# Kernel optimization log

Hardware: AMD Instinct MI355X
Metric: run time of the kernel (lower is better)

## Reference

```python
import jax, jax.numpy as jnp
import numpy as np

EMBED = 768
HEADS = 12
HEAD_DIM = EMBED // HEADS
HIDDEN = 4 * EMBED


def layer_norm(x, gamma, beta, eps=1e-5):
    mu = jnp.mean(x, axis=-1, keepdims=True)
    var = jnp.var(x, axis=-1, keepdims=True)
    return (x - mu) * jax.lax.rsqrt(var + eps) * gamma + beta


def setup_inputs() -> dict:
    key = jax.random.key(0)
    ks = jax.random.split(key, 10)
    B, N, C = 64, 577, EMBED
    s_in = 1.0 / np.sqrt(C)
    s_hid = 1.0 / np.sqrt(HIDDEN)
    return {
        "x": jax.random.normal(ks[0], (B, N, C), jnp.float32),
        "ln1_g": jnp.ones((C,), jnp.float32),
        "ln1_b": jnp.zeros((C,), jnp.float32),
        "w_qkv": jax.random.normal(ks[1], (C, 3 * C), jnp.float32) * s_in,  # no bias (qkv_bias=False)
        "w_proj": jax.random.normal(ks[2], (C, C), jnp.float32) * s_in,
        "b_proj": jnp.zeros((C,), jnp.float32),
        "ln2_g": jnp.ones((C,), jnp.float32),
        "ln2_b": jnp.zeros((C,), jnp.float32),
        "w_fc1": jax.random.normal(ks[3], (C, HIDDEN), jnp.float32) * s_in,
        "b_fc1": jnp.zeros((HIDDEN,), jnp.float32),
        "w_fc2": jax.random.normal(ks[4], (HIDDEN, C), jnp.float32) * s_hid,
        "b_fc2": jnp.zeros((C,), jnp.float32),
    }


def reference(x, ln1_g, ln1_b, w_qkv, w_proj, b_proj, ln2_g, ln2_b, w_fc1, b_fc1, w_fc2, b_fc2):
    B, N, C = x.shape
    # --- attention branch (pre-norm) ---
    h = layer_norm(x, ln1_g, ln1_b)
    qkv = (h @ w_qkv).reshape(B, N, 3, HEADS, HEAD_DIM)
    q = jnp.transpose(qkv[:, :, 0], (0, 2, 1, 3))  # [B,H,N,D]
    k = jnp.transpose(qkv[:, :, 1], (0, 2, 1, 3))
    v = jnp.transpose(qkv[:, :, 2], (0, 2, 1, 3))
    scale = HEAD_DIM ** -0.5
    att = jax.nn.softmax(jnp.einsum("bhnd,bhmd->bhnm", q, k) * scale, axis=-1)
    o = jnp.einsum("bhnm,bhmd->bhnd", att, v)
    o = jnp.transpose(o, (0, 2, 1, 3)).reshape(B, N, C)
    x = x + (o @ w_proj + b_proj)
    # --- MLP branch (pre-norm) ---
    h = layer_norm(x, ln2_g, ln2_b)
    h = jax.nn.gelu(h @ w_fc1 + b_fc1, approximate=False)
    x = x + (h @ w_fc2 + b_fc2)
    return x
```

## Files before the change

kernel.cpp:

```cpp
#include <hip/hip_runtime.h>
#include <hip/hip_bf16.h>
#include <math.h>

using bf16 = __hip_bfloat16;
typedef __attribute__((ext_vector_type(8))) short short8;
typedef __attribute__((ext_vector_type(4))) float f32x4;

#define NSEQ   577
#define NBATCH 64
#define NTOK   36928
#define NHEADS 12
#define HDIM   64
#define NP     640
#define CEMB   768
#define CHID   3072
#define NBH    (NBATCH*NHEADS)

__device__ __forceinline__ bf16 f2bf(float v){ return __float2bfloat16(v); }

__device__ __forceinline__ float gelu_f(float x) {
    float x3 = x * x * x;
    float y = 1.5957691216057308f * (x + 0.044715f * x3);
    float e = __expf(y);
    float t = 1.0f - 2.0f / (e + 1.0f);
    return 0.5f * x * (1.0f + t);
}

#define GLOAD_LDS16(gaddr, laddr) \
  __builtin_amdgcn_global_load_lds((__attribute__((address_space(1))) const void*)(gaddr), \
                                   (__attribute__((address_space(3))) void*)(laddr), 16, 0, 0)

__global__ __launch_bounds__(256) void transpose_w(const float* __restrict__ src,
                                                   bf16* __restrict__ dst, int R, int C) {
    long idx = (long)blockIdx.x * 256 + threadIdx.x;
    long total = (long)R * C;
    if (idx < total) {
        int r = (int)(idx / C);
        int c = (int)(idx - (long)r * C);
        dst[(long)c * R + r] = f2bf(src[idx]);
    }
}

__global__ __launch_bounds__(256) void ln_kernel(const float* __restrict__ x,
                                                 const float* __restrict__ gamma,
                                                 const float* __restrict__ beta,
                                                 bf16* __restrict__ out) {
    int row = blockIdx.x;
    const float* xr = x + (size_t)row * CEMB;
    int tid = threadIdx.x;
    float v0 = xr[tid], v1 = xr[tid + 256], v2 = xr[tid + 512];
    float s = v0 + v1 + v2;
    #pragma unroll
    for (int o = 32; o > 0; o >>= 1) s += __shfl_down(s, o);
    __shared__ float red[4];
    if ((tid & 63) == 0) red[tid >> 6] = s;
    __syncthreads();
    float mean = (red[0] + red[1] + red[2] + red[3]) * (1.0f / CEMB);
    float d0 = v0 - mean, d1 = v1 - mean, d2 = v2 - mean;
    float q = d0*d0 + d1*d1 + d2*d2;
    #pragma unroll
    for (int o = 32; o > 0; o >>= 1) q += __shfl_down(q, o);
    __shared__ float red2[4];
    if ((tid & 63) == 0) red2[tid >> 6] = q;
    __syncthreads();
    float var = (red2[0] + red2[1] + red2[2] + red2[3]) * (1.0f / CEMB);
    float rs = rsqrtf(var + 1e-5f);
    bf16* orow = out + (size_t)row * CEMB;
    orow[tid]       = f2bf(d0 * rs * gamma[tid]       + beta[tid]);
    orow[tid + 256] = f2bf(d1 * rs * gamma[tid + 256] + beta[tid + 256]);
    orow[tid + 512] = f2bf(d2 * rs * gamma[tid + 512] + beta[tid + 512]);
}

__global__ __launch_bounds__(256) void flash_attn(const bf16* __restrict__ qg,
                                                  const bf16* __restrict__ kg,
                                                  const bf16* __restrict__ vtg,
                                                  bf16* __restrict__ og) {
    const int tid = threadIdx.x, lane = tid & 63, w = tid >> 6;
    const int fr = lane & 15, fh = lane >> 4;
    const int bh = blockIdx.y;
    const int q0 = blockIdx.x * 128;
    const int wr = w * 32;

    __shared__ bf16 Ks[64 * 64];
    __shared__ bf16 Vs[64 * 64];
    __shared__ bf16 Ps[128 * 64];

    const bf16* qb = qg  + (size_t)bh * NP * HDIM;
    const bf16* kb = kg  + (size_t)bh * NP * HDIM;
    const bf16* vb = vtg + (size_t)bh * HDIM * NP;

    short8 qa[2][2];
    #pragma unroll
    for (int mi = 0; mi < 2; mi++)
        #pragma unroll
        for (int ks = 0; ks < 2; ks++)
            qa[mi][ks] = *reinterpret_cast<const short8*>(
                qb + (size_t)(q0 + wr + mi * 16 + fr) * HDIM + ks * 32 + fh * 8);

    f32x4 od[2][4] = {};
    float m_run[2][4], l_run[2][4];
    #pragma unroll
    for (int mi = 0; mi < 2; mi++)
        #pragma unroll
        for (int r = 0; r < 4; r++) { m_run[mi][r] = -1e30f; l_run[mi][r] = 0.f; }

    for (int t = 0; t < NP / 64; t++) {
        const int kb0 = t * 64;
        __syncthreads();
        {
            const bf16* src = kb + (size_t)kb0 * HDIM;
            GLOAD_LDS16(src + w * 512 + lane * 8,        Ks + w * 512);
            GLOAD_LDS16(src + 2048 + w * 512 + lane * 8, Ks + 2048 + w * 512);
        }
        {
            int d0 = w * 8;
            GLOAD_LDS16(vb + (size_t)(d0 + (lane >> 3)) * NP + kb0 + (lane & 7) * 8,
                        Vs + d0 * 64);
            d0 = 32 + w * 8;
            GLOAD_LDS16(vb + (size_t)(d0 + (lane >> 3)) * NP + kb0 + (lane & 7) * 8,
                        Vs + d0 * 64);
        }
        __syncthreads();

        f32x4 sacc[2][4] = {};
        short8 kf[4][2];
        #pragma unroll
        for (int n = 0; n < 4; n++)
            #pragma unroll
            for (int ks = 0; ks < 2; ks++)
                kf[n][ks] = *reinterpret_cast<const short8*>(&Ks[(n * 16 + fr) * 64 + ks * 32 + fh * 8]);
        #pragma unroll
        for (int mi = 0; mi < 2; mi++)
            #pragma unroll
            for (int n = 0; n < 4; n++)
                #pragma unroll
                for (int ks = 0; ks < 2; ks++)
                    sacc[mi][n] = __builtin_amdgcn_mfma_f32_16x16x32_bf16(qa[mi][ks], kf[n][ks], sacc[mi][n], 0, 0, 0);

        #pragma unroll
        for (int mi = 0; mi < 2; mi++) {
            float sv[4][4];
            float tm[4] = {-1e30f, -1e30f, -1e30f, -1e30f};
            #pragma unroll
            for (int n = 0; n < 4; n++) {
                int col = kb0 + n * 16 + fr;
                bool valid = col < NSEQ;
                #pragma unroll
                for (int r = 0; r < 4; r++) {
                    float s = sacc[mi][n][r] * 0.125f;
                    sv[n][r] = valid ? s : -1e30f;
                    tm[r] = fmaxf(tm[r], sv[n][r]);
                }
            }
            #pragma unroll
            for (int r = 0; r < 4; r++) {
                #pragma unroll
                for (int o = 1; o < 16; o <<= 1) tm[r] = fmaxf(tm[r], __shfl_xor(tm[r], o));
                float mn = fmaxf(m_run[mi][r], tm[r]);
                float sc = __expf(m_run[mi][r] - mn);
                m_run[mi][r] = mn;
                float ps = 0.f;
                #pragma unroll
                for (int n = 0; n < 4; n++) {
                    float e = __expf(sv[n][r] - mn);
                    sv[n][r] = e; ps += e;
                }
                #pragma unroll
                for (int o = 1; o < 16; o <<= 1) ps += __shfl_xor(ps, o);
                l_run[mi][r] = l_run[mi][r] * sc + ps;
                #pragma unroll
                for (int n2 = 0; n2 < 4; n2++) od[mi][n2][r] *= sc;
            }
            #pragma unroll
            for (int n = 0; n < 4; n++)
                #pragma unroll
                for (int r = 0; r < 4; r++)
                    Ps[(wr + mi * 16 + fh * 4 + r) * 64 + n * 16 + fr] = f2bf(sv[n][r]);
        }
        __syncthreads();

        short8 pa[2][2], vf[4][2];
        #pragma unroll
        for (int mi = 0; mi < 2; mi++)
            #pragma unroll
            for (int ks = 0; ks < 2; ks++)
                pa[mi][ks] = *reinterpret_cast<const short8*>(&Ps[(wr + mi * 16 + fr) * 64 + ks * 32 + fh * 8]);
        #pragma unroll
        for (int n2 = 0; n2 < 4; n2++)
            #pragma unroll
            for (int ks = 0; ks < 2; ks++)
                vf[n2][ks] = *reinterpret_cast<const short8*>(&Vs[(n2 * 16 + fr) * 64 + ks * 32 + fh * 8]);
        #pragma unroll
        for (int mi = 0; mi < 2; mi++)
            #pragma unroll
            for (int n2 = 0; n2 < 4; n2++)
                #pragma unroll
                for (int ks = 0; ks < 2; ks++)
                    od[mi][n2] = __builtin_amdgcn_mfma_f32_16x16x32_bf16(pa[mi][ks], vf[n2][ks], od[mi][n2], 0, 0, 0);
    }

    const int b = bh / NHEADS, hh = bh - b * NHEADS;
    #pragma unroll
    for (int mi = 0; mi < 2; mi++)
        #pragma unroll
        for (int r = 0; r < 4; r++) {
            int qrow = q0 + wr + mi * 16 + fh * 4 + r;
            if (qrow < NSEQ) {
                float inv = 1.f / l_run[mi][r];
                #pragma unroll
                for (int n2 = 0; n2 < 4; n2++)
                    og[((size_t)(b * NSEQ + qrow)) * CEMB + hh * HDIM + n2 * 16 + fr] =
                        f2bf(od[mi][n2][r] * inv);
            }
        }
}

#define MODE_QKV  1
#define MODE_PROJ 3
#define MODE_FC1  4
#define MODE_FC2  5

struct GemmParams {
    const bf16* A;
    const bf16* Bt;
    int M, N, K;
    int Mreal;
    float* Cf;
    bf16* Cb;
    const float* bias;
    const float* resid;
    bf16* qb; bf16* kb; bf16* vtb;
};

template<int MODE>
__global__ __launch_bounds__(256) void gemm128(GemmParams p) {
    __shared__ bf16 AsBuf[2][128 * 32];
    __shared__ bf16 BsBuf[2][128 * 32];
    const int tid  = threadIdx.x;
    const int lane = tid & 63;
    const int w    = tid >> 6;

    const int gx = gridDim.x, gy = gridDim.y;
    const int nwg = gx * gy;
    const int orig = blockIdx.y * gx + blockIdx.x;
    const int q8 = nwg >> 3, r8 = nwg & 7;
    const int xcd = orig & 7, oid = orig >> 3;
    const int lin2 = ((xcd < r8) ? xcd * (q8 + 1) : r8 * (q8 + 1) + (xcd - r8) * q8) + oid;
    const int bm = (lin2 / gy) * 128;
    const int bn = (lin2 % gy) * 128;

    const int Kd = p.K;
    const int wr = (w >> 1) * 64;
    const int wc = (w & 1) * 64;
    const int fr = lane & 15;
    const int fk = (lane >> 4) * 8;
    const int idx0 = w * 64 + lane;
    const int idx1 = idx0 + 256;
    const int r0 = idx0 >> 2, c0 = (idx0 & 3) * 8;
    const int r1 = idx1 >> 2, c1 = (idx1 & 3) * 8;

    const bf16* aS0 = p.A  + (size_t)(bm + r0) * Kd + c0;
    const bf16* aS1 = p.A  + (size_t)(bm + r1) * Kd + c1;
    const bf16* bS0 = p.Bt + (size_t)(bn + r0) * Kd + c0;
    const bf16* bS1 = p.Bt + (size_t)(bn + r1) * Kd + c1;

    f32x4 acc[4][4] = {};

    bf16 *Ac = AsBuf[0], *An = AsBuf[1];
    bf16 *Bc = BsBuf[0], *Bn = BsBuf[1];

    auto stage = [&](bf16* Ad, bf16* Bd) {
        GLOAD_LDS16(aS0, Ad + (size_t)w * 512);
        GLOAD_LDS16(aS1, Ad + (size_t)(w + 4) * 512);
        GLOAD_LDS16(bS0, Bd + (size_t)w * 512);
        GLOAD_LDS16(bS1, Bd + (size_t)(w + 4) * 512);
        aS0 += 32; aS1 += 32; bS0 += 32; bS1 += 32;
    };
    auto compute = [&](const bf16* Ad, const bf16* Bd) {
        short8 a[4], b[4];
        #pragma unroll
        for (int m = 0; m < 4; m++)
            a[m] = *reinterpret_cast<const short8*>(&Ad[(wr + m * 16 + fr) * 32 + fk]);
        #pragma unroll
        for (int n = 0; n < 4; n++)
            b[n] = *reinterpret_cast<const short8*>(&Bd[(wc + n * 16 + fr) * 32 + fk]);
        #pragma unroll
        for (int m = 0; m < 4; m++)
            #pragma unroll
            for (int n = 0; n < 4; n++)
                acc[m][n] = __builtin_amdgcn_mfma_f32_16x16x32_bf16(a[m], b[n], acc[m][n], 0, 0, 0);
    };

    const int T = Kd >> 5;
    stage(Ac, Bc);
    __syncthreads();
    for (int t = 1; t < T; ++t) {
        stage(An, Bn);
        compute(Ac, Bc);
        __syncthreads();
        bf16* tp;
        tp = Ac; Ac = An; An = tp;
        tp = Bc; Bc = Bn; Bn = tp;
    }
    compute(Ac, Bc);

    const int fq = (lane >> 4) * 4;
    const int colw = bn + wc;

    if (MODE == MODE_QKV) {
        const int which = colw / CEMB;
        const int hh = (colw - which * CEMB) >> 6;
        #pragma unroll
        for (int m = 0; m < 4; m++)
        #pragma unroll
        for (int r = 0; r < 4; r++) {
            int row = bm + wr + m * 16 + fq + r;
            if (row < p.Mreal) {
                int b2 = row / NSEQ;
                int n2 = row - b2 * NSEQ;
                size_t bh = (size_t)b2 * NHEADS + hh;
                if (which == 0) {
                    bf16* dst = p.qb + (bh * NP + n2) * HDIM + fr;
                    #pragma unroll
                    for (int n = 0; n < 4; n++) dst[n * 16] = f2bf(acc[m][n][r]);
                } else if (which == 1) {
                    bf16* dst = p.kb + (bh * NP + n2) * HDIM + fr;
                    #pragma unroll
                    for (int n = 0; n < 4; n++) dst[n * 16] = f2bf(acc[m][n][r]);
                } else {
                    bf16* dst = p.vtb + (bh * HDIM + fr) * NP + n2;
                    #pragma unroll
                    for (int n = 0; n < 4; n++) dst[(size_t)n * 16 * NP] = f2bf(acc[m][n][r]);
                }
            }
        }
    } else if (MODE == MODE_FC1) {
        const float* bp = p.bias + colw + fr;
        float bb[4];
        #pragma unroll
        for (int n = 0; n < 4; n++) bb[n] = bp[n * 16];
        #pragma unroll
        for (int m = 0; m < 4; m++)
        #pragma unroll
        for (int r = 0; r < 4; r++) {
            int row = bm + wr + m * 16 + fq + r;
            if (row < p.Mreal) {
                bf16* crow = p.Cb + (size_t)row * p.N + colw + fr;
                #pragma unroll
                for (int n = 0; n < 4; n++)
                    crow[n * 16] = f2bf(gelu_f(acc[m][n][r] + bb[n]));
            }
        }
    } else {
        const float* bp = p.bias + colw + fr;
        float bb[4];
        #pragma unroll
        for (int n = 0; n < 4; n++) bb[n] = bp[n * 16];
        #pragma unroll
        for (int m = 0; m < 4; m++)
        #pragma unroll
        for (int r = 0; r < 4; r++) {
            int row = bm + wr + m * 16 + fq + r;
            if (row < p.Mreal) {
                float* crow = p.Cf + (size_t)row * p.N + colw + fr;
                const float* rrow = p.resid + (size_t)row * p.N + colw + fr;
                #pragma unroll
                for (int n = 0; n < 4; n++)
                    crow[n * 16] = acc[m][n][r] + bb[n] + rrow[n * 16];
            }
        }
    }
}

extern "C" void kernel_launch(void* const* d_in, const int* in_sizes, int n_in,
                              void* d_out, int out_size, void* d_ws, size_t ws_size,
                              hipStream_t stream) {
    const float* x      = (const float*)d_in[0];
    const float* ln1_g  = (const float*)d_in[1];
    const float* ln1_b  = (const float*)d_in[2];
    const float* w_qkv  = (const float*)d_in[3];
    const float* w_proj = (const float*)d_in[4];
    const float* b_proj = (const float*)d_in[5];
    const float* ln2_g  = (const float*)d_in[6];
    const float* ln2_b  = (const float*)d_in[7];
    const float* w_fc1  = (const float*)d_in[8];
    const float* b_fc1  = (const float*)d_in[9];
    const float* w_fc2  = (const float*)d_in[10];
    const float* b_fc2  = (const float*)d_in[11];
    float* out = (float*)d_out;

    char* ws = (char*)d_ws;
    auto al = [](size_t b){ return (b + 255) & ~(size_t)255; };
    size_t off = 0;
    auto take = [&](size_t b)->char* { char* p = ws + off; off += al(b); return p; };

    bf16* wqkvT  = (bf16*)take((size_t)2304 * 768 * 2);
    bf16* wprojT = (bf16*)take((size_t)768 * 768 * 2);
    bf16* wfc1T  = (bf16*)take((size_t)3072 * 768 * 2);
    bf16* wfc2T  = (bf16*)take((size_t)768 * 3072 * 2);
    bf16* h      = (bf16*)take((size_t)(NTOK + 128) * CEMB * 2);
    bf16* o      = (bf16*)take((size_t)(NTOK + 128) * CEMB * 2);
    size_t fixedEnd = off;

    const size_t qkvB = (size_t)NBH * NP * HDIM * 2;
    bf16* q_c  = (bf16*)(ws + fixedEnd);
    bf16* k_c  = (bf16*)(ws + fixedEnd + qkvB);
    bf16* vT_c = (bf16*)(ws + fixedEnd + 2 * qkvB);
    bf16* g_c  = (bf16*)(ws + fixedEnd);

    transpose_w<<<(768 * 2304 + 255) / 256, 256, 0, stream>>>(w_qkv, wqkvT, 768, 2304);
    transpose_w<<<(768 * 768 + 255) / 256, 256, 0, stream>>>(w_proj, wprojT, 768, 768);
    transpose_w<<<(768 * 3072 + 255) / 256, 256, 0, stream>>>(w_fc1, wfc1T, 768, 3072);
    transpose_w<<<(3072 * 768 + 255) / 256, 256, 0, stream>>>(w_fc2, wfc2T, 3072, 768);

    ln_kernel<<<NTOK, 256, 0, stream>>>(x, ln1_g, ln1_b, h);

    {
        const int mPad = (NTOK + 127) & ~127;
        GemmParams p{};
        p.A = h; p.Bt = wqkvT;
        p.M = mPad; p.N = 3 * CEMB; p.K = CEMB; p.Mreal = NTOK;
        p.qb = q_c; p.kb = k_c; p.vtb = vT_c;
        gemm128<MODE_QKV><<<dim3(mPad / 128, 3 * CEMB / 128), 256, 0, stream>>>(p);
    }

    flash_attn<<<dim3(NP / 128, NBH), 256, 0, stream>>>(q_c, k_c, vT_c, o);

    {
        const int mPad = (NTOK + 127) & ~127;
        GemmParams p{};
        p.A = o; p.Bt = wprojT;
        p.M = mPad; p.N = CEMB; p.K = CEMB; p.Mreal = NTOK;
        p.Cf = out; p.bias = b_proj; p.resid = x;
        gemm128<MODE_PROJ><<<dim3(mPad / 128, CEMB / 128), 256, 0, stream>>>(p);
    }

    ln_kernel<<<NTOK, 256, 0, stream>>>(out, ln2_g, ln2_b, h);

    {
        const int mPad = (NTOK + 127) & ~127;
        GemmParams p{};
        p.A = h; p.Bt = wfc1T;
        p.M = mPad; p.N = CHID; p.K = CEMB; p.Mreal = NTOK;
        p.Cb = g_c; p.bias = b_fc1;
        gemm128<MODE_FC1><<<dim3(mPad / 128, CHID / 128), 256, 0, stream>>>(p);
    }

    {
        const int mPad = (NTOK + 127) & ~127;
        GemmParams p{};
        p.A = g_c; p.Bt = wfc2T;
        p.M = mPad; p.N = CEMB; p.K = CHID; p.Mreal = NTOK;
        p.Cf = out; p.bias = b_fc2; p.resid = out;
        gemm128<MODE_FC2><<<dim3(mPad / 128, CEMB / 128), 256, 0, stream>>>(p);
    }
}
```

Measured before the change: 1.404 ms.

## Enlarge GEMM tiles to 256x256x64 with 8 waves and fold attention scale into Q

Replaces the 128x128x32 GEMM with a 256x256 tile, K-step 64, and 512 threads. Each wave now computes a 128x64 sub-tile, which raises arithmetic intensity per LDS and global load. The attention scale of 0.125 moves into the QKV epilogue for Q, removing a multiply per score in flash attention. The trade-offs are 128KB of LDS per block, a larger accumulator register footprint, fewer blocks for the N=768 GEMMs, and more padded rows with M padded to 37120.

Measured after the change: 1.377 ms. No clear change (-2.0%).

```diff
diff --git a/kernel.cpp b/kernel.cpp
--- a/kernel.cpp
+++ b/kernel.cpp
@@ -9,6 +9,7 @@
 #define NSEQ   577
 #define NBATCH 64
 #define NTOK   36928
+#define MPAD   37120
 #define NHEADS 12
 #define HDIM   64
 #define NP     640
@@ -147,7 +148,7 @@
                 bool valid = col < NSEQ;
                 #pragma unroll
                 for (int r = 0; r < 4; r++) {
-                    float s = sacc[mi][n][r] * 0.125f;
+                    float s = sacc[mi][n][r];
                     sv[n][r] = valid ? s : -1e30f;
                     tm[r] = fmaxf(tm[r], sv[n][r]);
                 }
@@ -233,9 +234,9 @@
 };
 
 template<int MODE>
-__global__ __launch_bounds__(256) void gemm128(GemmParams p) {
-    __shared__ bf16 AsBuf[2][128 * 32];
-    __shared__ bf16 BsBuf[2][128 * 32];
+__global__ __launch_bounds__(512, 2) void gemm256(GemmParams p) {
+    __shared__ bf16 AsBuf[2][256 * 64];
+    __shared__ bf16 BsBuf[2][256 * 64];
     const int tid  = threadIdx.x;
     const int lane = tid & 63;
     const int w    = tid >> 6;
@@ -246,52 +247,53 @@
     const int q8 = nwg >> 3, r8 = nwg & 7;
     const int xcd = orig & 7, oid = orig >> 3;
     const int lin2 = ((xcd < r8) ? xcd * (q8 + 1) : r8 * (q8 + 1) + (xcd - r8) * q8) + oid;
-    const int bm = (lin2 / gy) * 128;
-    const int bn = (lin2 % gy) * 128;
+    const int bm = (lin2 / gy) * 256;
+    const int bn = (lin2 % gy) * 256;
 
     const int Kd = p.K;
-    const int wr = (w >> 1) * 64;
-    const int wc = (w & 1) * 64;
+    const int wm = w >> 2, wn = w & 3;
+    const int wr = wm * 128, wc = wn * 64;
     const int fr = lane & 15;
     const int fk = (lane >> 4) * 8;
-    const int idx0 = w * 64 + lane;
-    const int idx1 = idx0 + 256;
-    const int r0 = idx0 >> 2, c0 = (idx0 & 3) * 8;
-    const int r1 = idx1 >> 2, c1 = (idx1 & 3) * 8;
-
-    const bf16* aS0 = p.A  + (size_t)(bm + r0) * Kd + c0;
-    const bf16* aS1 = p.A  + (size_t)(bm + r1) * Kd + c1;
-    const bf16* bS0 = p.Bt + (size_t)(bn + r0) * Kd + c0;
-    const bf16* bS1 = p.Bt + (size_t)(bn + r1) * Kd + c1;
-
-    f32x4 acc[4][4] = {};
-
-    bf16 *Ac = AsBuf[0], *An = AsBuf[1];
-    bf16 *Bc = BsBuf[0], *Bn = BsBuf[1];
+
+    const int sr = w * 8 + (lane >> 3);
+    const int sc = (lane & 7) * 8;
+    const bf16* aS[4]; const bf16* bS[4];
+    #pragma unroll
+    for (int s = 0; s < 4; s++) {
+        aS[s] = p.A  + (size_t)(bm + s * 64 + sr) * Kd + sc;
+        bS[s] = p.Bt + (size_t)(bn + s * 64 + sr) * Kd + sc;
+    }
+
+    f32x4 acc[8][4] = {};
+    bf16 *Ac = AsBuf[0], *An = AsBuf[1], *Bc = BsBuf[0], *Bn = BsBuf[1];
 
     auto stage = [&](bf16* Ad, bf16* Bd) {
-        GLOAD_LDS16(aS0, Ad + (size_t)w * 512);
-        GLOAD_LDS16(aS1, Ad + (size_t)(w + 4) * 512);
-        GLOAD_LDS16(bS0, Bd + (size_t)w * 512);
-        GLOAD_LDS16(bS1, Bd + (size_t)(w + 4) * 512);
-        aS0 += 32; aS1 += 32; bS0 += 32; bS1 += 32;
+        #pragma unroll
+        for (int s = 0; s < 4; s++) {
+            GLOAD_LDS16(aS[s], Ad + (size_t)(s * 8 + w) * 512);
+            GLOAD_LDS16(bS[s], Bd + (size_t)(s * 8 + w) * 512);
+            aS[s] += 64; bS[s] += 64;
+        }
     };
     auto compute = [&](const bf16* Ad, const bf16* Bd) {
-        short8 a[4], b[4];
-        #pragma unroll
-        for (int m = 0; m < 4; m++)
-            a[m] = *reinterpret_cast<const short8*>(&Ad[(wr + m * 16 + fr) * 32 + fk]);
-        #pragma unroll
-        for (int n = 0; n < 4; n++)
-            b[n] = *reinterpret_cast<const short8*>(&Bd[(wc + n * 16 + fr) * 32 + fk]);
-        #pragma unroll
-        for (int m = 0; m < 4; m++)
+        #pragma unroll
+        for (int ks = 0; ks < 2; ks++) {
+            short8 b[4];
             #pragma unroll
             for (int n = 0; n < 4; n++)
-                acc[m][n] = __builtin_amdgcn_mfma_f32_16x16x32_bf16(a[m], b[n], acc[m][n], 0, 0, 0);
+                b[n] = *reinterpret_cast<const short8*>(&Bd[(wc + n * 16 + fr) * 64 + ks * 32 + fk]);
+            #pragma unroll
+            for (int m = 0; m < 8; m++) {
+                short8 a = *reinterpret_cast<const short8*>(&Ad[(wr + m * 16 + fr) * 64 + ks * 32 + fk]);
+                #pragma unroll
+                for (int n = 0; n < 4; n++)
+                    acc[m][n] = __builtin_amdgcn_mfma_f32_16x16x32_bf16(a, b[n], acc[m][n], 0, 0, 0);
+            }
+        }
     };
 
-    const int T = Kd >> 5;
+    const int T = Kd >> 6;
     stage(Ac, Bc);
     __syncthreads();
     for (int t = 1; t < T; ++t) {
@@ -310,8 +312,9 @@
     if (MODE == MODE_QKV) {
         const int which = colw / CEMB;
         const int hh = (colw - which * CEMB) >> 6;
-        #pragma unroll
-        for (int m = 0; m < 4; m++)
+        const float scl = (which == 0) ? 0.125f : 1.0f;
+        #pragma unroll
+        for (int m = 0; m < 8; m++)
         #pragma unroll
         for (int r = 0; r < 4; r++) {
             int row = bm + wr + m * 16 + fq + r;
@@ -322,7 +325,7 @@
                 if (which == 0) {
                     bf16* dst = p.qb + (bh * NP + n2) * HDIM + fr;
                     #pragma unroll
-                    for (int n = 0; n < 4; n++) dst[n * 16] = f2bf(acc[m][n][r]);
+                    for (int n = 0; n < 4; n++) dst[n * 16] = f2bf(acc[m][n][r] * scl);
                 } else if (which == 1) {
                     bf16* dst = p.kb + (bh * NP + n2) * HDIM + fr;
                     #pragma unroll
@@ -340,7 +343,7 @@
         #pragma unroll
         for (int n = 0; n < 4; n++) bb[n] = bp[n * 16];
         #pragma unroll
-        for (int m = 0; m < 4; m++)
+        for (int m = 0; m < 8; m++)
         #pragma unroll
         for (int r = 0; r < 4; r++) {
             int row = bm + wr + m * 16 + fq + r;
@@ -357,7 +360,7 @@
         #pragma unroll
         for (int n = 0; n < 4; n++) bb[n] = bp[n * 16];
         #pragma unroll
-        for (int m = 0; m < 4; m++)
+        for (int m = 0; m < 8; m++)
         #pragma unroll
         for (int r = 0; r < 4; r++) {
             int row = bm + wr + m * 16 + fq + r;
@@ -398,8 +401,8 @@
     bf16* wprojT = (bf16*)take((size_t)768 * 768 * 2);
     bf16* wfc1T  = (bf16*)take((size_t)3072 * 768 * 2);
     bf16* wfc2T  = (bf16*)take((size_t)768 * 3072 * 2);
-    bf16* h      = (bf16*)take((size_t)(NTOK + 128) * CEMB * 2);
-    bf16* o      = (bf16*)take((size_t)(NTOK + 128) * CEMB * 2);
+    bf16* h      = (bf16*)take((size_t)MPAD * CEMB * 2);
+    bf16* o      = (bf16*)take((size_t)MPAD * CEMB * 2);
     size_t fixedEnd = off;
 
     const size_t qkvB = (size_t)NBH * NP * HDIM * 2;
@@ -416,42 +419,38 @@
     ln_kernel<<<NTOK, 256, 0, stream>>>(x, ln1_g, ln1_b, h);
 
     {
-        const int mPad = (NTOK + 127) & ~127;
         GemmParams p{};
         p.A = h; p.Bt = wqkvT;
-        p.M = mPad; p.N = 3 * CEMB; p.K = CEMB; p.Mreal = NTOK;
+        p.M = MPAD; p.N = 3 * CEMB; p.K = CEMB; p.Mreal = NTOK;
         p.qb = q_c; p.kb = k_c; p.vtb = vT_c;
-        gemm128<MODE_QKV><<<dim3(mPad / 128, 3 * CEMB / 128), 256, 0, stream>>>(p);
+        gemm256<MODE_QKV><<<dim3(MPAD / 256, 3 * CEMB / 256), 512, 0, stream>>>(p);
     }
 
     flash_attn<<<dim3(NP / 128, NBH), 256, 0, stream>>>(q_c, k_c, vT_c, o);
 
     {
-        const int mPad = (NTOK + 127) & ~127;
         GemmParams p{};
         p.A = o; p.Bt = wprojT;
-        p.M = mPad; p.N = CEMB; p.K = CEMB; p.Mreal = NTOK;
+        p.M = MPAD; p.N = CEMB; p.K = CEMB; p.Mreal = NTOK;
         p.Cf = out; p.bias = b_proj; p.resid = x;
-        gemm128<MODE_PROJ><<<dim3(mPad / 128, CEMB / 128), 256, 0, stream>>>(p);
+        gemm256<MODE_PROJ><<<dim3(MPAD / 256, CEMB / 256), 512, 0, stream>>>(p);
     }
 
     ln_kernel<<<NTOK, 256, 0, stream>>>(out, ln2_g, ln2_b, h);
 
     {
-        const int mPad = (NTOK + 127) & ~127;
         GemmParams p{};
         p.A = h; p.Bt = wfc1T;
-        p.M = mPad; p.N = CHID; p.K = CEMB; p.Mreal = NTOK;
+        p.M = MPAD; p.N = CHID; p.K = CEMB; p.Mreal = NTOK;
         p.Cb = g_c; p.bias = b_fc1;
-        gemm128<MODE_FC1><<<dim3(mPad / 128, CHID / 128), 256, 0, stream>>>(p);
+        gemm256<MODE_FC1><<<dim3(MPAD / 256, CHID / 256), 512, 0, stream>>>(p);
     }
 
     {
-        const int mPad = (NTOK + 127) & ~127;
         GemmParams p{};
         p.A = g_c; p.Bt = wfc2T;
-        p.M = mPad; p.N = CEMB; p.K = CHID; p.Mreal = NTOK;
+        p.M = MPAD; p.N = CEMB; p.K = CHID; p.Mreal = NTOK;
         p.Cf = out; p.bias = b_fc2; p.resid = out;
-        gemm128<MODE_FC2><<<dim3(mPad / 128, CEMB / 128), 256, 0, stream>>>(p);
-    }
-}
+        gemm256<MODE_FC2><<<dim3(MPAD / 256, CEMB / 256), 512, 0, stream>>>(p);
+    }
+}
```
